# Kernel tuning notes

Hardware: AMD Instinct MI355X
Metric: run time of the kernel (lower is better)

The kernel has to match this reference:

```python
import jax, jax.numpy as jnp
import numpy as np

KS = 3        # kernel_size == stride (non-overlapping patches)
ALPHA = 0.1


def setup_inputs() -> dict:
    key = jax.random.key(0)
    k1, k2, k3 = jax.random.split(key, 3)
    b, c, m, n = 32, 256, 56, 56
    l = (m - KS) // KS + 1   # 18
    kk = (n - KS) // KS + 1  # 18
    activation = jax.random.normal(k1, (b, c, m, n), dtype=jnp.float32)
    # precomputed bernoulli(0.5) draws (0/1), kept as int so they are constants
    rc = jax.random.randint(k2, (b, c, m, n), 0, 2, dtype=jnp.int32)
    p_patch_mask = jax.random.randint(k3, (b, c, l, kk), 0, 2, dtype=jnp.int32)
    return {"activation": activation, "rc": rc, "p_patch_mask": p_patch_mask}


def reference(activation, rc, p_patch_mask):
    b, c, m, n = activation.shape
    l, k = p_patch_mask.shape[2], p_patch_mask.shape[3]
    dt = activation.dtype

    # per-(b,c) spatial peak -> [b,c,1,1]
    peak = jnp.max(activation, axis=(2, 3), keepdims=True)
    pc = (activation == peak).astype(dt)          # peak indicator
    bc_dash = rc.astype(dt) * pc                  # rc * pc (peak dropout mask)

    # broadcast patch-level bernoulli mask to pixel level over covered region
    full = jnp.repeat(jnp.repeat(p_patch_mask.astype(dt), KS, axis=2), KS, axis=3)
    # uncovered border (fold leaves it zero) -> pad with zeros to (m, n)
    full = jnp.pad(full, ((0, 0), (0, 0), (0, m - l * KS), (0, n - k * KS)))
    # zero-out patch mask at peak locations (bc_dd_batch[activation==peak]=0)
    bc_dd = full * (1.0 - pc)

    bc = bc_dash + bc_dd
    return jnp.where(bc >= 1.0, activation * ALPHA, activation)
```

## Files before the change

kernel.cpp:

```cpp
#include <hip/hip_runtime.h>
#include <math.h>

#define KS     3
#define ALPHA  0.1f
#define M      56
#define N      56
#define L      18
#define KK     18
#define PIX    (M * N)
#define VEC    (PIX / 4)
#define NTHR   256
#define COVER  (L * KS)

__device__ __forceinline__ float4 process4(float4 x, int v, float peak, size_t base,
                                           const int* __restrict__ rc,
                                           const int* smask) {
    const int p0 = v * 4;
    const int i  = p0 / N;
    const int j0 = p0 - i * N;
    const bool inrow = (i < COVER);
    const int  mrow  = (i / 3) * KK;

    float vals[4] = {x.x, x.y, x.z, x.w};
    float o[4];
#pragma unroll
    for (int e = 0; e < 4; ++e) {
        const float a = vals[e];
        const int   j = j0 + e;
        bool cond;
        if (a == peak) {
            cond = (rc[base + (size_t)(p0 + e)] != 0);
        } else {
            cond = inrow && (j < COVER) && (smask[mrow + j / 3] != 0);
        }
        o[e] = cond ? a * ALPHA : a;
    }
    return make_float4(o[0], o[1], o[2], o[3]);
}

__global__ __launch_bounds__(NTHR) void div_block_kernel(
    const float* __restrict__ act,
    const int*   __restrict__ rc,
    const int*   __restrict__ pmask,
    float*       __restrict__ out) {

    const int    plane = blockIdx.x;
    const int    tid   = threadIdx.x;
    const size_t base  = (size_t)plane * PIX;

    const float4* a4 = (const float4*)(act + base);
    float4*       o4 = (float4*)(out + base);

    __shared__ int   smask[L * KK];
    __shared__ float wmax[NTHR / 64];
    __shared__ float peak_s;

    for (int s = tid; s < L * KK; s += NTHR)
        smask[s] = pmask[(size_t)plane * (L * KK) + s];

    const int v0 = tid, v1 = tid + NTHR, v2 = tid + 2 * NTHR, v3 = tid + 3 * NTHR;
    float4 x0 = a4[v0];
    float4 x1 = a4[v1];
    float4 x2 = a4[v2];
    const bool has3 = (v3 < VEC);
    float4 x3 = has3 ? a4[v3]
                     : make_float4(-INFINITY, -INFINITY, -INFINITY, -INFINITY);

    float lmax = fmaxf(fmaxf(x0.x, x0.y), fmaxf(x0.z, x0.w));
    lmax = fmaxf(lmax, fmaxf(fmaxf(x1.x, x1.y), fmaxf(x1.z, x1.w)));
    lmax = fmaxf(lmax, fmaxf(fmaxf(x2.x, x2.y), fmaxf(x2.z, x2.w)));
    lmax = fmaxf(lmax, fmaxf(fmaxf(x3.x, x3.y), fmaxf(x3.z, x3.w)));

#pragma unroll
    for (int off = 32; off > 0; off >>= 1)
        lmax = fmaxf(lmax, __shfl_xor(lmax, off, 64));
    if ((tid & 63) == 0)
        wmax[tid >> 6] = lmax;
    __syncthreads();
    if (tid == 0)
        peak_s = fmaxf(fmaxf(wmax[0], wmax[1]), fmaxf(wmax[2], wmax[3]));
    __syncthreads();
    const float peak = peak_s;

    o4[v0] = process4(x0, v0, peak, base, rc, smask);
    o4[v1] = process4(x1, v1, peak, base, rc, smask);
    o4[v2] = process4(x2, v2, peak, base, rc, smask);
    if (has3)
        o4[v3] = process4(x3, v3, peak, base, rc, smask);
}

extern "C" void kernel_launch(void* const* d_in, const int* in_sizes, int n_in,
                              void* d_out, int out_size, void* d_ws, size_t ws_size,
                              hipStream_t stream) {
    const float* act   = (const float*)d_in[0];
    const int*   rc    = (const int*)d_in[1];
    const int*   pmask = (const int*)d_in[2];
    float*       out   = (float*)d_out;

    const int planes = in_sizes[0] / PIX;
    div_block_kernel<<<planes, NTHR, 0, stream>>>(act, rc, pmask, out);
}
```

Before: 39.97 us.

## Map one wavefront per plane, dropping block barriers, with nontemporal stores

Each 64-lane wavefront now handles a whole 56x56 plane, and a block carries four planes. The peak reduction becomes a pure wave shuffle, so the shared-memory cross-wave step and both __syncthreads are gone. Each lane now holds 13 float4 loads in flight, and output writes use nontemporal stores. The cost is higher register pressure and a quarter as many blocks (2048 instead of 8192), which may reduce latency hiding.

```diff
diff --git a/kernel.cpp b/kernel.cpp
--- a/kernel.cpp
+++ b/kernel.cpp
@@ -9,84 +9,107 @@
 #define KK     18
 #define PIX    (M * N)
 #define VEC    (PIX / 4)
-#define NTHR   256
+#define WAVES  4
+#define NTHR   (WAVES * 64)
 #define COVER  (L * KS)
 
-__device__ __forceinline__ float4 process4(float4 x, int v, float peak, size_t base,
-                                           const int* __restrict__ rc,
-                                           const int* smask) {
+typedef float vf4 __attribute__((ext_vector_type(4)));
+
+__device__ __forceinline__ float rmax4(vf4 x) {
+    return fmaxf(fmaxf(x.x, x.y), fmaxf(x.z, x.w));
+}
+
+__device__ __forceinline__ vf4 proc4(vf4 x, int v, float peak, size_t base,
+                                     const int* __restrict__ rc,
+                                     const int* sm) {
     const int p0 = v * 4;
-    const int i  = p0 / N;
+    const int i  = v / 14;
     const int j0 = p0 - i * N;
     const bool inrow = (i < COVER);
     const int  mrow  = (i / 3) * KK;
 
-    float vals[4] = {x.x, x.y, x.z, x.w};
-    float o[4];
+    vf4 o;
 #pragma unroll
     for (int e = 0; e < 4; ++e) {
-        const float a = vals[e];
+        const float a = x[e];
         const int   j = j0 + e;
         bool cond;
         if (a == peak) {
             cond = (rc[base + (size_t)(p0 + e)] != 0);
         } else {
-            cond = inrow && (j < COVER) && (smask[mrow + j / 3] != 0);
+            cond = inrow && (j < COVER) && (sm[mrow + j / 3] != 0);
         }
         o[e] = cond ? a * ALPHA : a;
     }
-    return make_float4(o[0], o[1], o[2], o[3]);
+    return o;
 }
 
 __global__ __launch_bounds__(NTHR) void div_block_kernel(
     const float* __restrict__ act,
     const int*   __restrict__ rc,
     const int*   __restrict__ pmask,
-    float*       __restrict__ out) {
+    float*       __restrict__ out,
+    int planes) {
 
-    const int    plane = blockIdx.x;
-    const int    tid   = threadIdx.x;
-    const size_t base  = (size_t)plane * PIX;
+    const int tid = threadIdx.x;
+    const int w   = tid >> 6;
+    const int l   = tid & 63;
+    const int plane = blockIdx.x * WAVES + w;
+    if (plane >= planes) return;
 
-    const float4* a4 = (const float4*)(act + base);
-    float4*       o4 = (float4*)(out + base);
+    const size_t base = (size_t)plane * PIX;
+    const vf4* a4 = (const vf4*)(act + base);
+    vf4*       o4 = (vf4*)(out + base);
 
-    __shared__ int   smask[L * KK];
-    __shared__ float wmax[NTHR / 64];
-    __shared__ float peak_s;
+    __shared__ int smask[WAVES][L * KK];
+    int* sm = smask[w];
+    for (int s = l; s < L * KK; s += 64)
+        sm[s] = pmask[(size_t)plane * (L * KK) + s];
 
-    for (int s = tid; s < L * KK; s += NTHR)
-        smask[s] = pmask[(size_t)plane * (L * KK) + s];
+    vf4 x0  = a4[l];
+    vf4 x1  = a4[l + 1 * 64];
+    vf4 x2  = a4[l + 2 * 64];
+    vf4 x3  = a4[l + 3 * 64];
+    vf4 x4  = a4[l + 4 * 64];
+    vf4 x5  = a4[l + 5 * 64];
+    vf4 x6  = a4[l + 6 * 64];
+    vf4 x7  = a4[l + 7 * 64];
+    vf4 x8  = a4[l + 8 * 64];
+    vf4 x9  = a4[l + 9 * 64];
+    vf4 x10 = a4[l + 10 * 64];
+    vf4 x11 = a4[l + 11 * 64];
+    const bool has12 = (l < (VEC - 12 * 64));
+    vf4 x12;
+    if (has12) x12 = a4[l + 12 * 64];
+    else       x12 = (vf4){-INFINITY, -INFINITY, -INFINITY, -INFINITY};
 
-    const int v0 = tid, v1 = tid + NTHR, v2 = tid + 2 * NTHR, v3 = tid + 3 * NTHR;
-    float4 x0 = a4[v0];
-    float4 x1 = a4[v1];
-    float4 x2 = a4[v2];
-    const bool has3 = (v3 < VEC);
-    float4 x3 = has3 ? a4[v3]
-                     : make_float4(-INFINITY, -INFINITY, -INFINITY, -INFINITY);
-
-    float lmax = fmaxf(fmaxf(x0.x, x0.y), fmaxf(x0.z, x0.w));
-    lmax = fmaxf(lmax, fmaxf(fmaxf(x1.x, x1.y), fmaxf(x1.z, x1.w)));
-    lmax = fmaxf(lmax, fmaxf(fmaxf(x2.x, x2.y), fmaxf(x2.z, x2.w)));
-    lmax = fmaxf(lmax, fmaxf(fmaxf(x3.x, x3.y), fmaxf(x3.z, x3.w)));
-
+    float m0 = fmaxf(rmax4(x0),  rmax4(x1));
+    float m1 = fmaxf(rmax4(x2),  rmax4(x3));
+    float m2 = fmaxf(rmax4(x4),  rmax4(x5));
+    float m3 = fmaxf(rmax4(x6),  rmax4(x7));
+    float m4 = fmaxf(rmax4(x8),  rmax4(x9));
+    float m5 = fmaxf(rmax4(x10), rmax4(x11));
+    float mx = fmaxf(fmaxf(fmaxf(m0, m1), fmaxf(m2, m3)),
+                     fmaxf(fmaxf(m4, m5), rmax4(x12)));
 #pragma unroll
     for (int off = 32; off > 0; off >>= 1)
-        lmax = fmaxf(lmax, __shfl_xor(lmax, off, 64));
-    if ((tid & 63) == 0)
-        wmax[tid >> 6] = lmax;
-    __syncthreads();
-    if (tid == 0)
-        peak_s = fmaxf(fmaxf(wmax[0], wmax[1]), fmaxf(wmax[2], wmax[3]));
-    __syncthreads();
-    const float peak = peak_s;
+        mx = fmaxf(mx, __shfl_xor(mx, off, 64));
+    const float peak = mx;
 
-    o4[v0] = process4(x0, v0, peak, base, rc, smask);
-    o4[v1] = process4(x1, v1, peak, base, rc, smask);
-    o4[v2] = process4(x2, v2, peak, base, rc, smask);
-    if (has3)
-        o4[v3] = process4(x3, v3, peak, base, rc, smask);
+    __builtin_nontemporal_store(proc4(x0,  l,           peak, base, rc, sm), &o4[l]);
+    __builtin_nontemporal_store(proc4(x1,  l + 1 * 64,  peak, base, rc, sm), &o4[l + 1 * 64]);
+    __builtin_nontemporal_store(proc4(x2,  l + 2 * 64,  peak, base, rc, sm), &o4[l + 2 * 64]);
+    __builtin_nontemporal_store(proc4(x3,  l + 3 * 64,  peak, base, rc, sm), &o4[l + 3 * 64]);
+    __builtin_nontemporal_store(proc4(x4,  l + 4 * 64,  peak, base, rc, sm), &o4[l + 4 * 64]);
+    __builtin_nontemporal_store(proc4(x5,  l + 5 * 64,  peak, base, rc, sm), &o4[l + 5 * 64]);
+    __builtin_nontemporal_store(proc4(x6,  l + 6 * 64,  peak, base, rc, sm), &o4[l + 6 * 64]);
+    __builtin_nontemporal_store(proc4(x7,  l + 7 * 64,  peak, base, rc, sm), &o4[l + 7 * 64]);
+    __builtin_nontemporal_store(proc4(x8,  l + 8 * 64,  peak, base, rc, sm), &o4[l + 8 * 64]);
+    __builtin_nontemporal_store(proc4(x9,  l + 9 * 64,  peak, base, rc, sm), &o4[l + 9 * 64]);
+    __builtin_nontemporal_store(proc4(x10, l + 10 * 64, peak, base, rc, sm), &o4[l + 10 * 64]);
+    __builtin_nontemporal_store(proc4(x11, l + 11 * 64, peak, base, rc, sm), &o4[l + 11 * 64]);
+    if (has12)
+        __builtin_nontemporal_store(proc4(x12, l + 12 * 64, peak, base, rc, sm), &o4[l + 12 * 64]);
 }
 
 extern "C" void kernel_launch(void* const* d_in, const int* in_sizes, int n_in,
@@ -98,5 +121,6 @@
     float*       out   = (float*)d_out;
 
     const int planes = in_sizes[0] / PIX;
-    div_block_kernel<<<planes, NTHR, 0, stream>>>(act, rc, pmask, out);
+    const int blocks = (planes + WAVES - 1) / WAVES;
+    div_block_kernel<<<blocks, NTHR, 0, stream>>>(act, rc, pmask, out, planes);
 }
```

Measured after the change: 41.65 us. 1.04x slower.
